# Kernel optimization log

Hardware: AMD Instinct MI355X
Metric: run time of the kernel (lower is better)

Reference implementation:

```python
import jax, jax.numpy as jnp
import numpy as np

HEADS = 16
DIM = 1024
HEAD_DIM = DIM // HEADS


def setup_inputs() -> dict:
    key = jax.random.key(0)
    k1, k2 = jax.random.split(key)
    images = jax.random.normal(k1, (2, 2048, DIM), dtype=jnp.float32)
    # torch nn.Linear(dim, 3*dim, bias=False): y = x @ W.T, W: [3*dim, dim].
    # Store as [dim, 3*dim] for direct x @ W_qkv.
    W_qkv = jax.random.normal(k2, (DIM, 3 * DIM), dtype=jnp.float32) / np.sqrt(DIM)
    return {"images": images, "W_qkv": W_qkv}


def reference(images, W_qkv):
    B, S, D = images.shape
    qkv = images @ W_qkv  # [B, S, 3D]
    q, k, v = jnp.split(qkv, 3, axis=-1)
    # [B, S, H, Dh] -> [B, H, S, Dh]
    def to_heads(t):
        return t.reshape(B, S, HEADS, HEAD_DIM).transpose(0, 2, 1, 3)
    q, k, v = to_heads(q), to_heads(k), to_heads(v)
    scale = 1.0 / jnp.sqrt(jnp.asarray(HEAD_DIM, dtype=q.dtype))
    scores = jnp.einsum('bhqd,bhkd->bhqk', q, k) * scale  # [B, H, S, S]
    probs = jax.nn.softmax(scores, axis=-1)
    out = jnp.einsum('bhqk,bhkd->bhqd', probs, v)  # [B, H, S, Dh]
    return out.transpose(0, 2, 1, 3).reshape(B, S, D)
```

## Files before the change

kernel.cpp:

```cpp
#include <hip/hip_runtime.h>
#include <hip/hip_bf16.h>
#include <math.h>

typedef __bf16 bf16x8 __attribute__((ext_vector_type(8)));
typedef float f32x4 __attribute__((ext_vector_type(4)));
typedef unsigned short u16x8 __attribute__((ext_vector_type(8)));
typedef _Float16 h16x4 __attribute__((ext_vector_type(4)));
typedef unsigned short u16;

#define S_LEN 2048
#define DMODEL 1024
#define NH 16
#define NROWS 65536

__device__ __forceinline__ u16 f2bf(float f) {
    __bf16 b = (__bf16)f;
    return __builtin_bit_cast(u16, b);
}
__device__ __forceinline__ float bf2f(u16 u) {
    union { unsigned int i; float f; } v; v.i = ((unsigned int)u) << 16; return v.f;
}

__device__ __forceinline__ void gload16(const u16* g, u16* lds_base) {
    __builtin_amdgcn_global_load_lds(
        (const __attribute__((address_space(1))) unsigned int*)g,
        (__attribute__((address_space(3))) unsigned int*)lds_base,
        16, 0, 0);
}

__global__ __launch_bounds__(256) void cvt_x(const float* __restrict__ in, u16* __restrict__ outp) {
    int i = (blockIdx.x * 256 + threadIdx.x) * 4;
    float4 v = *(const float4*)(in + i);
    outp[i + 0] = f2bf(v.x); outp[i + 1] = f2bf(v.y);
    outp[i + 2] = f2bf(v.z); outp[i + 3] = f2bf(v.w);
}

__global__ __launch_bounds__(256) void transpose_w(const float* __restrict__ W, u16* __restrict__ Wt) {
    __shared__ u16 tile[32][33];
    int n0 = blockIdx.x * 32, k0 = blockIdx.y * 32;
    int tx = threadIdx.x & 31, ty = threadIdx.x >> 5;
#pragma unroll
    for (int i = 0; i < 4; i++) {
        int k = ty + i * 8;
        tile[k][tx] = f2bf(W[(size_t)(k0 + k) * 3072 + n0 + tx]);
    }
    __syncthreads();
#pragma unroll
    for (int i = 0; i < 4; i++) {
        int n = ty + i * 8;
        Wt[(size_t)(n0 + n) * 1024 + k0 + tx] = tile[tx][n];
    }
}

__global__ __launch_bounds__(256) void qkv_gemm(const u16* __restrict__ A, const u16* __restrict__ Bt,
                                                u16* __restrict__ C) {
    __shared__ alignas(16) u16 As[128 * 64];
    __shared__ alignas(16) u16 Bs[128 * 64];
    const int tid = threadIdx.x, l = tid & 63, w = tid >> 6;
    const int bm = blockIdx.y, bn = blockIdx.x;
    const int wm = w >> 1, wn = w & 1;
    const int c0 = l & 15, g = l >> 4;
    f32x4 acc[4][4] = {};
    for (int kt = 0; kt < 1024; kt += 64) {
        __syncthreads();
#pragma unroll
        for (int n = 0; n < 4; n++) {
            int i = tid + n * 256;
            int r = i >> 3, c = i & 7;
            int cs = c ^ (r & 7);
            u16* dstA = As + (size_t)(w * 64 + n * 256) * 8;
            u16* dstB = Bs + (size_t)(w * 64 + n * 256) * 8;
            gload16(A + (size_t)(bm * 128 + r) * 1024 + kt + cs * 8, dstA);
            gload16(Bt + (size_t)(bn * 128 + r) * 1024 + kt + cs * 8, dstB);
        }
        __syncthreads();
#pragma unroll
        for (int kk = 0; kk < 2; kk++) {
            bf16x8 af[4], bfr[4];
#pragma unroll
            for (int m = 0; m < 4; m++) {
                int row = wm * 64 + m * 16 + c0;
                af[m] = *(const bf16x8*)((const char*)As + row * 128 + (((g + kk * 4) ^ (row & 7)) << 4));
            }
#pragma unroll
            for (int n = 0; n < 4; n++) {
                int row = wn * 64 + n * 16 + c0;
                bfr[n] = *(const bf16x8*)((const char*)Bs + row * 128 + (((g + kk * 4) ^ (row & 7)) << 4));
            }
#pragma unroll
            for (int m = 0; m < 4; m++)
#pragma unroll
                for (int n = 0; n < 4; n++)
                    acc[m][n] = __builtin_amdgcn_mfma_f32_16x16x32_bf16(af[m], bfr[n], acc[m][n], 0, 0, 0);
        }
    }
#pragma unroll
    for (int m = 0; m < 4; m++)
#pragma unroll
        for (int n = 0; n < 4; n++)
#pragma unroll
            for (int j = 0; j < 4; j++) {
                int row = bm * 128 + wm * 64 + m * 16 + 4 * g + j;
                int col = bn * 128 + wn * 64 + n * 16 + c0;
                C[(size_t)row * 3072 + col] = f2bf(acc[m][n][j]);
            }
}

__global__ __launch_bounds__(256) void transpose_v(const u16* __restrict__ QKV, u16* __restrict__ Vtp) {
    __shared__ u16 tile[64][72];
    const int bh = blockIdx.x >> 5, st = blockIdx.x & 31;
    const int b = bh >> 4, h = bh & 15;
    const u16* src = QKV + (size_t)b * S_LEN * 3072 + 2048 + h * 64;
    const int sl = threadIdx.x >> 2;
    const int cg = (threadIdx.x & 3) * 16;
#pragma unroll
    for (int ii = 0; ii < 2; ii++) {
        u16x8 v = *(const u16x8*)(src + (size_t)(st * 64 + sl) * 3072 + cg + ii * 8);
        *(u16x8*)&tile[sl][cg + ii * 8] = v;
    }
    __syncthreads();
    const int dl = threadIdx.x >> 2;
#pragma unroll
    for (int ii = 0; ii < 2; ii++) {
        u16x8 o;
#pragma unroll
        for (int q = 0; q < 8; q++) {
            int p = cg + ii * 8 + q;
            int kb = 2 * (p >> 5) + ((p >> 2) & 1);
            int t = kb * 16 + ((p >> 3) & 3) * 4 + (p & 3);
            o[q] = tile[t][dl];
        }
        *(u16x8*)(Vtp + ((size_t)bh * 64 + dl) * S_LEN + st * 64 + cg + ii * 8) = o;
    }
}

__global__ __launch_bounds__(256, 4) void attn9(const u16* __restrict__ QKV, const u16* __restrict__ Vtp,
                                                float* __restrict__ outp, _Float16* __restrict__ Op1,
                                                float* __restrict__ Mp, float* __restrict__ Lp) {
    __shared__ alignas(16) u16 Ks[2][64 * 64];
    __shared__ alignas(16) u16 Vs[2][64 * 64];
    const int bid = blockIdx.x;
    const int wg = ((bid & 7) << 8) | (bid >> 3);
    const int tid = threadIdx.x, l = tid & 63, w = tid >> 6;
    const int bh = wg >> 6, rest = wg & 63;
    const int qt = rest >> 1, hf = rest & 1;
    const int b = bh >> 4, h = bh & 15;
    const int c0 = l & 15, g = l >> 4;
    const u16* Qb = QKV + (size_t)b * S_LEN * 3072 + h * 64;
    const u16* Kb = Qb + 1024;
    const u16* Vb = Vtp + (size_t)bh * 64 * S_LEN;
    const int kv0 = hf * 1024;
    const int qrow = qt * 64 + w * 16 + c0;

    const int r0 = tid >> 3, cs0 = (tid & 7) ^ (r0 & 7);
    const int i1 = tid + 256, r1 = i1 >> 3, cs1 = (i1 & 7) ^ (r1 & 7);
    const int dbA = (w * 64) * 8, dbB = (256 + w * 64) * 8;

    int off[8];
#pragma unroll
    for (int x = 0; x < 4; x++)
#pragma unroll
        for (int kk = 0; kk < 2; kk++)
            off[x * 2 + kk] = (x * 16 + c0) * 128 + (((g + 4 * kk) ^ (c0 & 7)) << 4);

    bf16x8 qf[2];
    {
        const float qs = 0.125f * 1.44269504f;
#pragma unroll
        for (int kk = 0; kk < 2; kk++) {
            u16x8 v = *(const u16x8*)(Qb + (size_t)qrow * 3072 + kk * 32 + g * 8);
            bf16x8 q;
#pragma unroll
            for (int j = 0; j < 8; j++) q[j] = (__bf16)(bf2f(v[j]) * qs);
            qf[kk] = q;
        }
    }
    bf16x8 vone;
#pragma unroll
    for (int j = 0; j < 8; j++) vone[j] = (__bf16)1.0f;

    float m_r = 0.f;
    f32x4 accO[4] = {};
    f32x4 accL = {};

    gload16(Kb + (size_t)(kv0 + r0) * 3072 + cs0 * 8, Ks[0] + dbA);
    gload16(Kb + (size_t)(kv0 + r1) * 3072 + cs1 * 8, Ks[0] + dbB);
    gload16(Vb + (size_t)r0 * S_LEN + kv0 + cs0 * 8, Vs[0] + dbA);
    gload16(Vb + (size_t)r1 * S_LEN + kv0 + cs1 * 8, Vs[0] + dbB);

    for (int t = 0; t < 16; t++) {
        const int cur = t & 1;
        __syncthreads();
        if (t + 1 < 16) {
            const int kvn = kv0 + (t + 1) * 64;
            gload16(Kb + (size_t)(kvn + r0) * 3072 + cs0 * 8, Ks[cur ^ 1] + dbA);
            gload16(Kb + (size_t)(kvn + r1) * 3072 + cs1 * 8, Ks[cur ^ 1] + dbB);
            gload16(Vb + (size_t)r0 * S_LEN + kvn + cs0 * 8, Vs[cur ^ 1] + dbA);
            gload16(Vb + (size_t)r1 * S_LEN + kvn + cs1 * 8, Vs[cur ^ 1] + dbB);
        }
        const char* Kc = (const char*)Ks[cur];
        const char* Vc = (const char*)Vs[cur];
        f32x4 sc[4];
        const float nm = -m_r;
#pragma unroll
        for (int kb = 0; kb < 4; kb++) { sc[kb][0] = nm; sc[kb][1] = nm; sc[kb][2] = nm; sc[kb][3] = nm; }
        __builtin_amdgcn_s_setprio(1);
#pragma unroll
        for (int kb = 0; kb < 4; kb++)
#pragma unroll
            for (int kk = 0; kk < 2; kk++) {
                bf16x8 kf = *(const bf16x8*)(Kc + off[kb * 2 + kk]);
                sc[kb] = __builtin_amdgcn_mfma_f32_16x16x32_bf16(kf, qf[kk], sc[kb], 0, 0, 0);
            }
        __builtin_amdgcn_s_setprio(0);
        bf16x8 vf[2][4];
#pragma unroll
        for (int kk = 0; kk < 2; kk++)
#pragma unroll
            for (int n = 0; n < 4; n++)
                vf[kk][n] = *(const bf16x8*)(Vc + off[n * 2 + kk]);
        float m0 = fmaxf(fmaxf(sc[0][0], sc[0][1]), sc[0][2]);
        float m1 = fmaxf(fmaxf(sc[0][3], sc[1][0]), sc[1][1]);
        float m2 = fmaxf(fmaxf(sc[1][2], sc[1][3]), sc[2][0]);
        float m3 = fmaxf(fmaxf(sc[2][1], sc[2][2]), sc[2][3]);
        float m4 = fmaxf(fmaxf(sc[3][0], sc[3][1]), sc[3][2]);
        float mx = fmaxf(fmaxf(fmaxf(m0, m1), m2), fmaxf(fmaxf(m3, m4), sc[3][3]));
        if (!__all(mx <= 8.f)) {
            float mxr = fmaxf(mx, __shfl_xor(mx, 16));
            mxr = fmaxf(mxr, __shfl_xor(mxr, 32));
            float adj = fmaxf(mxr, 0.f);
            float alpha = __builtin_amdgcn_exp2f(-adj);
            m_r += adj;
#pragma unroll
            for (int j = 0; j < 4; j++) {
                float aj = __shfl(alpha, 20 * g + j);
                accL[j] *= aj;
#pragma unroll
                for (int n = 0; n < 4; n++) accO[n][j] *= aj;
            }
#pragma unroll
            for (int kb = 0; kb < 4; kb++)
#pragma unroll
                for (int j = 0; j < 4; j++) sc[kb][j] -= adj;
        }
#pragma unroll
        for (int kb = 0; kb < 4; kb++)
#pragma unroll
            for (int j = 0; j < 4; j++)
                sc[kb][j] = __builtin_amdgcn_exp2f(sc[kb][j]);
        __builtin_amdgcn_s_setprio(1);
#pragma unroll
        for (int kk = 0; kk < 2; kk++) {
            bf16x8 pf;
#pragma unroll
            for (int j = 0; j < 4; j++) {
                pf[j]     = (__bf16)sc[2 * kk][j];
                pf[j + 4] = (__bf16)sc[2 * kk + 1][j];
            }
            accL = __builtin_amdgcn_mfma_f32_16x16x32_bf16(pf, vone, accL, 0, 0, 0);
#pragma unroll
            for (int n = 0; n < 4; n++)
                accO[n] = __builtin_amdgcn_mfma_f32_16x16x32_bf16(pf, vf[kk][n], accO[n], 0, 0, 0);
        }
        __builtin_amdgcn_s_setprio(0);
    }
    const int rowbase = qt * 64 + w * 16;
    const int rowg0 = bh * 2048 + rowbase;
    if (hf == 0) {
#pragma unroll
        for (int j = 0; j < 4; j++) {
            float inv = 1.0f / accL[j];
            int row = rowbase + 4 * g + j;
            float* op = outp + ((size_t)b * S_LEN + row) * DMODEL + h * 64;
#pragma unroll
            for (int n = 0; n < 4; n++) op[n * 16 + c0] = accO[n][j] * inv;
        }
    } else {
#pragma unroll
        for (int j = 0; j < 4; j++) {
            float inv = 1.0f / accL[j];
            size_t rg = (size_t)(rowg0 + 4 * g + j) * 64;
#pragma unroll
            for (int n = 0; n < 4; n++) Op1[rg + n * 16 + c0] = (_Float16)(accO[n][j] * inv);
        }
    }
    if (g == 0) Mp[hf * NROWS + rowg0 + c0] = m_r;
    if (c0 == 0) {
#pragma unroll
        for (int j = 0; j < 4; j++) Lp[hf * NROWS + rowg0 + 4 * g + j] = accL[j];
    }
}

__global__ __launch_bounds__(256) void attn_merge(float* __restrict__ outp, const _Float16* __restrict__ Op1,
                                                  const float* __restrict__ Mp, const float* __restrict__ Lp) {
    int t = blockIdx.x * 256 + threadIdx.x;
    int r = t >> 2;
    int dc = (t & 3) * 16;
    int bh = r >> 11, srow = r & 2047;
    int b = bh >> 4, h = bh & 15;
    float m0 = Mp[r], m1 = Mp[NROWS + r];
    float l0 = Lp[r], l1 = Lp[NROWS + r];
    float M = fmaxf(m0, m1);
    float w0 = __builtin_amdgcn_exp2f(m0 - M) * l0;
    float w1 = __builtin_amdgcn_exp2f(m1 - M) * l1;
    float inv = 1.0f / (w0 + w1);
    float a0 = w0 * inv, a1 = w1 * inv;
    float* op = outp + ((size_t)b * S_LEN + srow) * DMODEL + h * 64 + dc;
    const _Float16* o1 = Op1 + (size_t)r * 64 + dc;
#pragma unroll
    for (int q = 0; q < 4; q++) {
        float4 v0 = *(const float4*)(op + q * 4);
        h16x4 v1 = *(const h16x4*)(o1 + q * 4);
        v0.x = a0 * v0.x + a1 * (float)v1[0];
        v0.y = a0 * v0.y + a1 * (float)v1[1];
        v0.z = a0 * v0.z + a1 * (float)v1[2];
        v0.w = a0 * v0.w + a1 * (float)v1[3];
        *(float4*)(op + q * 4) = v0;
    }
}

extern "C" void kernel_launch(void* const* d_in, const int* in_sizes, int n_in,
                              void* d_out, int out_size, void* d_ws, size_t ws_size,
                              hipStream_t stream) {
    const float* X = (const float*)d_in[0];
    const float* W = (const float*)d_in[1];
    float* out = (float*)d_out;

    u16* Xb  = (u16*)d_ws;
    u16* Wt  = Xb + (size_t)4096 * 1024;
    u16* QKV = Wt + (size_t)3072 * 1024;
    u16* Vtp = QKV + (size_t)4096 * 3072;
    _Float16* Op1 = (_Float16*)Xb;
    float* Mp = (float*)Wt;
    float* Lp = Mp + 2 * NROWS;

    cvt_x<<<4096, 256, 0, stream>>>(X, Xb);
    transpose_w<<<dim3(96, 32), 256, 0, stream>>>(W, Wt);
    qkv_gemm<<<dim3(24, 32), 256, 0, stream>>>(Xb, Wt, QKV);
    transpose_v<<<1024, 256, 0, stream>>>(QKV, Vtp);
    attn9<<<2048, 256, 0, stream>>>(QKV, Vtp, out, Op1, Mp, Lp);
    attn_merge<<<1024, 256, 0, stream>>>(out, Op1, Mp, Lp);
}
```

Baseline: 116.8 us.

## Merge split-KV attention halves in-block via LDS, drop separate merge kernel

```diff
diff --git a/kernel.cpp b/kernel.cpp
--- a/kernel.cpp
+++ b/kernel.cpp
@@ -5,13 +5,11 @@
 typedef __bf16 bf16x8 __attribute__((ext_vector_type(8)));
 typedef float f32x4 __attribute__((ext_vector_type(4)));
 typedef unsigned short u16x8 __attribute__((ext_vector_type(8)));
-typedef _Float16 h16x4 __attribute__((ext_vector_type(4)));
 typedef unsigned short u16;
 
 #define S_LEN 2048
 #define DMODEL 1024
 #define NH 16
-#define NROWS 65536
 
 __device__ __forceinline__ u16 f2bf(float f) {
     __bf16 b = (__bf16)f;
@@ -134,27 +132,27 @@
     }
 }
 
-__global__ __launch_bounds__(256, 4) void attn9(const u16* __restrict__ QKV, const u16* __restrict__ Vtp,
-                                                float* __restrict__ outp, _Float16* __restrict__ Op1,
-                                                float* __restrict__ Mp, float* __restrict__ Lp) {
-    __shared__ alignas(16) u16 Ks[2][64 * 64];
-    __shared__ alignas(16) u16 Vs[2][64 * 64];
+__global__ __launch_bounds__(512, 4) void attn11(const u16* __restrict__ QKV, const u16* __restrict__ Vtp,
+                                                 float* __restrict__ outp) {
+    __shared__ alignas(16) u16 Ks[2][2][64 * 64];
+    __shared__ alignas(16) u16 Vs[2][2][64 * 64];
     const int bid = blockIdx.x;
-    const int wg = ((bid & 7) << 8) | (bid >> 3);
+    const int wg = ((bid & 7) << 7) | (bid >> 3);
     const int tid = threadIdx.x, l = tid & 63, w = tid >> 6;
-    const int bh = wg >> 6, rest = wg & 63;
-    const int qt = rest >> 1, hf = rest & 1;
+    const int hf = w >> 2, wsub = w & 3;
+    const int qt = wg & 31, bh = wg >> 5;
     const int b = bh >> 4, h = bh & 15;
     const int c0 = l & 15, g = l >> 4;
     const u16* Qb = QKV + (size_t)b * S_LEN * 3072 + h * 64;
     const u16* Kb = Qb + 1024;
     const u16* Vb = Vtp + (size_t)bh * 64 * S_LEN;
     const int kv0 = hf * 1024;
-    const int qrow = qt * 64 + w * 16 + c0;
-
-    const int r0 = tid >> 3, cs0 = (tid & 7) ^ (r0 & 7);
-    const int i1 = tid + 256, r1 = i1 >> 3, cs1 = (i1 & 7) ^ (r1 & 7);
-    const int dbA = (w * 64) * 8, dbB = (256 + w * 64) * 8;
+    const int qrow = qt * 64 + wsub * 16 + c0;
+
+    const int tid_h = tid & 255;
+    const int r0 = tid_h >> 3, cs0 = (tid_h & 7) ^ (r0 & 7);
+    const int i1 = tid_h + 256, r1 = i1 >> 3, cs1 = (i1 & 7) ^ (r1 & 7);
+    const int dbA = (wsub * 64) * 8, dbB = (256 + wsub * 64) * 8;
 
     int off[8];
 #pragma unroll
@@ -183,23 +181,23 @@
     f32x4 accO[4] = {};
     f32x4 accL = {};
 
-    gload16(Kb + (size_t)(kv0 + r0) * 3072 + cs0 * 8, Ks[0] + dbA);
-    gload16(Kb + (size_t)(kv0 + r1) * 3072 + cs1 * 8, Ks[0] + dbB);
-    gload16(Vb + (size_t)r0 * S_LEN + kv0 + cs0 * 8, Vs[0] + dbA);
-    gload16(Vb + (size_t)r1 * S_LEN + kv0 + cs1 * 8, Vs[0] + dbB);
+    gload16(Kb + (size_t)(kv0 + r0) * 3072 + cs0 * 8, Ks[hf][0] + dbA);
+    gload16(Kb + (size_t)(kv0 + r1) * 3072 + cs1 * 8, Ks[hf][0] + dbB);
+    gload16(Vb + (size_t)r0 * S_LEN + kv0 + cs0 * 8, Vs[hf][0] + dbA);
+    gload16(Vb + (size_t)r1 * S_LEN + kv0 + cs1 * 8, Vs[hf][0] + dbB);
 
     for (int t = 0; t < 16; t++) {
         const int cur = t & 1;
         __syncthreads();
         if (t + 1 < 16) {
             const int kvn = kv0 + (t + 1) * 64;
-            gload16(Kb + (size_t)(kvn + r0) * 3072 + cs0 * 8, Ks[cur ^ 1] + dbA);
-            gload16(Kb + (size_t)(kvn + r1) * 3072 + cs1 * 8, Ks[cur ^ 1] + dbB);
-            gload16(Vb + (size_t)r0 * S_LEN + kvn + cs0 * 8, Vs[cur ^ 1] + dbA);
-            gload16(Vb + (size_t)r1 * S_LEN + kvn + cs1 * 8, Vs[cur ^ 1] + dbB);
-        }
-        const char* Kc = (const char*)Ks[cur];
-        const char* Vc = (const char*)Vs[cur];
+            gload16(Kb + (size_t)(kvn + r0) * 3072 + cs0 * 8, Ks[hf][cur ^ 1] + dbA);
+            gload16(Kb + (size_t)(kvn + r1) * 3072 + cs1 * 8, Ks[hf][cur ^ 1] + dbB);
+            gload16(Vb + (size_t)r0 * S_LEN + kvn + cs0 * 8, Vs[hf][cur ^ 1] + dbA);
+            gload16(Vb + (size_t)r1 * S_LEN + kvn + cs1 * 8, Vs[hf][cur ^ 1] + dbB);
+        }
+        const char* Kc = (const char*)Ks[hf][cur];
+        const char* Vc = (const char*)Vs[hf][cur];
         f32x4 sc[4];
         const float nm = -m_r;
 #pragma unroll
@@ -264,58 +262,39 @@
         }
         __builtin_amdgcn_s_setprio(0);
     }
-    const int rowbase = qt * 64 + w * 16;
-    const int rowg0 = bh * 2048 + rowbase;
+    __syncthreads();
+    float* Opart = (float*)&Ks[0][0][0];
+    float* m1s   = (float*)&Vs[0][0][0];
+    float* l1s   = m1s + 64;
+    if (hf == 1) {
+#pragma unroll
+        for (int j = 0; j < 4; j++) {
+            int rj = wsub * 16 + 4 * g + j;
+#pragma unroll
+            for (int n = 0; n < 4; n++) Opart[rj * 65 + n * 16 + c0] = accO[n][j];
+        }
+        if (g == 0) m1s[wsub * 16 + c0] = m_r;
+        if (c0 == 0) {
+#pragma unroll
+            for (int j = 0; j < 4; j++) l1s[wsub * 16 + 4 * g + j] = accL[j];
+        }
+    }
+    __syncthreads();
     if (hf == 0) {
 #pragma unroll
         for (int j = 0; j < 4; j++) {
-            float inv = 1.0f / accL[j];
-            int row = rowbase + 4 * g + j;
-            float* op = outp + ((size_t)b * S_LEN + row) * DMODEL + h * 64;
-#pragma unroll
-            for (int n = 0; n < 4; n++) op[n * 16 + c0] = accO[n][j] * inv;
-        }
-    } else {
-#pragma unroll
-        for (int j = 0; j < 4; j++) {
-            float inv = 1.0f / accL[j];
-            size_t rg = (size_t)(rowg0 + 4 * g + j) * 64;
-#pragma unroll
-            for (int n = 0; n < 4; n++) Op1[rg + n * 16 + c0] = (_Float16)(accO[n][j] * inv);
-        }
-    }
-    if (g == 0) Mp[hf * NROWS + rowg0 + c0] = m_r;
-    if (c0 == 0) {
-#pragma unroll
-        for (int j = 0; j < 4; j++) Lp[hf * NROWS + rowg0 + 4 * g + j] = accL[j];
-    }
-}
-
-__global__ __launch_bounds__(256) void attn_merge(float* __restrict__ outp, const _Float16* __restrict__ Op1,
-                                                  const float* __restrict__ Mp, const float* __restrict__ Lp) {
-    int t = blockIdx.x * 256 + threadIdx.x;
-    int r = t >> 2;
-    int dc = (t & 3) * 16;
-    int bh = r >> 11, srow = r & 2047;
-    int b = bh >> 4, h = bh & 15;
-    float m0 = Mp[r], m1 = Mp[NROWS + r];
-    float l0 = Lp[r], l1 = Lp[NROWS + r];
-    float M = fmaxf(m0, m1);
-    float w0 = __builtin_amdgcn_exp2f(m0 - M) * l0;
-    float w1 = __builtin_amdgcn_exp2f(m1 - M) * l1;
-    float inv = 1.0f / (w0 + w1);
-    float a0 = w0 * inv, a1 = w1 * inv;
-    float* op = outp + ((size_t)b * S_LEN + srow) * DMODEL + h * 64 + dc;
-    const _Float16* o1 = Op1 + (size_t)r * 64 + dc;
-#pragma unroll
-    for (int q = 0; q < 4; q++) {
-        float4 v0 = *(const float4*)(op + q * 4);
-        h16x4 v1 = *(const h16x4*)(o1 + q * 4);
-        v0.x = a0 * v0.x + a1 * (float)v1[0];
-        v0.y = a0 * v0.y + a1 * (float)v1[1];
-        v0.z = a0 * v0.z + a1 * (float)v1[2];
-        v0.w = a0 * v0.w + a1 * (float)v1[3];
-        *(float4*)(op + q * 4) = v0;
+            int rj = wsub * 16 + 4 * g + j;
+            float m1v = m1s[rj], l1v = l1s[rj];
+            float m0v = __shfl(m_r, 20 * g + j);
+            float M = fmaxf(m0v, m1v);
+            float a0 = __builtin_amdgcn_exp2f(m0v - M);
+            float a1 = __builtin_amdgcn_exp2f(m1v - M);
+            float inv = 1.0f / (a0 * accL[j] + a1 * l1v);
+            float* op = outp + ((size_t)b * S_LEN + qt * 64 + rj) * DMODEL + h * 64;
+#pragma unroll
+            for (int n = 0; n < 4; n++)
+                op[n * 16 + c0] = (a0 * accO[n][j] + a1 * Opart[rj * 65 + n * 16 + c0]) * inv;
+        }
     }
 }
 
@@ -330,14 +309,10 @@
     u16* Wt  = Xb + (size_t)4096 * 1024;
     u16* QKV = Wt + (size_t)3072 * 1024;
     u16* Vtp = QKV + (size_t)4096 * 3072;
-    _Float16* Op1 = (_Float16*)Xb;
-    float* Mp = (float*)Wt;
-    float* Lp = Mp + 2 * NROWS;
 
     cvt_x<<<4096, 256, 0, stream>>>(X, Xb);
     transpose_w<<<dim3(96, 32), 256, 0, stream>>>(W, Wt);
     qkv_gemm<<<dim3(24, 32), 256, 0, stream>>>(Xb, Wt, QKV);
     transpose_v<<<1024, 256, 0, stream>>>(QKV, Vtp);
-    attn9<<<2048, 256, 0, stream>>>(QKV, Vtp, out, Op1, Mp, Lp);
-    attn_merge<<<1024, 256, 0, stream>>>(out, Op1, Mp, Lp);
-}
+    attn11<<<1024, 512, 0, stream>>>(QKV, Vtp, out);
+}
```

Measured after the change: 107.2 us. -8.2%, faster.
